# Kernel optimization log

Hardware: AMD Instinct MI355X
Metric: run time of the kernel (lower is better)

## Reference

```python
import jax, jax.numpy as jnp
import numpy as np

DIM = 2048
N_HEADS = 16
N_KV_HEADS = 8
HEAD_DIM = DIM // N_HEADS  # 128
N_REP = N_HEADS // N_KV_HEADS  # 2
HIDDEN = 4 * DIM  # Project hidden dim
SEQ = 2048
BSZ = 2
ROPE_THETA = 10000.0
NEG_INF = -1e9


def setup_inputs() -> dict:
    key = jax.random.key(0)
    ks = jax.random.split(key, 10)
    s_in = 1.0 / np.sqrt(DIM)
    s_hid = 1.0 / np.sqrt(HIDDEN)
    x = jax.random.normal(ks[0], (BSZ, SEQ, DIM), jnp.float32)
    wq = jax.random.normal(ks[1], (DIM, N_HEADS * HEAD_DIM), jnp.float32) * s_in
    wk_w1 = jax.random.normal(ks[2], (DIM, HIDDEN), jnp.float32) * s_in
    wk_w2 = jax.random.normal(ks[3], (HIDDEN, N_KV_HEADS * HEAD_DIM), jnp.float32) * s_hid
    wk_w3 = jax.random.normal(ks[4], (DIM, HIDDEN), jnp.float32) * s_in
    wv_w1 = jax.random.normal(ks[5], (DIM, HIDDEN), jnp.float32) * s_in
    wv_w2 = jax.random.normal(ks[6], (HIDDEN, N_KV_HEADS * HEAD_DIM), jnp.float32) * s_hid
    wv_w3 = jax.random.normal(ks[7], (DIM, HIDDEN), jnp.float32) * s_in
    wo = jax.random.normal(ks[8], (N_HEADS * HEAD_DIM, DIM), jnp.float32) * s_in
    # RoPE tables: angle[t, j] = t * theta^(-2j/head_dim), j in [0, head_dim/2)
    inv_freq = 1.0 / (ROPE_THETA ** (np.arange(0, HEAD_DIM, 2, dtype=np.float64) / HEAD_DIM))
    ang = np.outer(np.arange(SEQ, dtype=np.float64), inv_freq)
    freqs_cos = jnp.asarray(np.cos(ang), jnp.float32)  # [SEQ, HEAD_DIM//2]
    freqs_sin = jnp.asarray(np.sin(ang), jnp.float32)
    # causal additive mask [1, 1, SEQ, SEQ]
    mask = jnp.triu(jnp.full((SEQ, SEQ), NEG_INF, jnp.float32), k=1)[None, None]
    return {
        "x": x, "wq": wq,
        "wk_w1": wk_w1, "wk_w2": wk_w2, "wk_w3": wk_w3,
        "wv_w1": wv_w1, "wv_w2": wv_w2, "wv_w3": wv_w3,
        "wo": wo, "freqs_cos": freqs_cos, "freqs_sin": freqs_sin,
        "mask": mask, "start_pos": 0,
    }


def _rope(x, cos, sin):
    # x: [b, s, h, d]; pairs (x[2j], x[2j+1]) rotated as complex multiply
    xr = x[..., 0::2]
    xi = x[..., 1::2]
    c = cos[None, :, None, :]
    s = sin[None, :, None, :]
    out_r = xr * c - xi * s
    out_i = xr * s + xi * c
    return jnp.stack([out_r, out_i], axis=-1).reshape(x.shape)


def _project(x, w1, w2, w3):
    # SwiGLU-style projection: w2(silu(x@w1) * (x@w3))
    return (jax.nn.silu(x @ w1) * (x @ w3)) @ w2


def reference(x, wq, wk_w1, wk_w2, wk_w3, wv_w1, wv_w2, wv_w3, wo,
              freqs_cos, freqs_sin, mask, start_pos):
    b, s, _ = x.shape
    q = (x @ wq).reshape(b, s, N_HEADS, HEAD_DIM)
    q = _rope(q, freqs_cos, freqs_sin)
    k = _project(x, wk_w1, wk_w2, wk_w3).reshape(b, s, N_KV_HEADS, HEAD_DIM)
    v = _project(x, wv_w1, wv_w2, wv_w3).reshape(b, s, N_KV_HEADS, HEAD_DIM)
    k = _rope(k, freqs_cos, freqs_sin)
    o_keys, o_values = k, v  # is_training=True path: cache is just current k/v
    # repeat_kv (GQA) -> [b, h, s, d]
    kr = jnp.repeat(k, N_REP, axis=2).transpose(0, 2, 1, 3)
    vr = jnp.repeat(v, N_REP, axis=2).transpose(0, 2, 1, 3)
    qt = q.transpose(0, 2, 1, 3)
    scores = jnp.einsum('bhqd,bhkd->bhqk', qt, kr) / np.sqrt(HEAD_DIM).astype(np.float32)
    scores = scores + mask
    attn = jax.nn.softmax(scores.astype(jnp.float32), axis=-1).astype(qt.dtype)
    out = jnp.einsum('bhqk,bhkd->bhqd', attn, vr)
    out = out.transpose(0, 2, 1, 3).reshape(b, s, N_HEADS * HEAD_DIM)
    return (out @ wo, o_keys, o_values)
```

## Files before the change

### kernel.cpp

```cpp
#include <hip/hip_runtime.h>

typedef unsigned short ushort_t;
typedef __attribute__((ext_vector_type(4))) float f32x4;
typedef __attribute__((ext_vector_type(8))) __bf16 bf16x8;
typedef __attribute__((ext_vector_type(4))) unsigned short ushort4_t;
typedef __attribute__((ext_vector_type(8))) unsigned short ushort8_t;
typedef __attribute__((ext_vector_type(2))) unsigned int u32x2;

#define AS1 __attribute__((address_space(1)))
#define AS3 __attribute__((address_space(3)))

__device__ __forceinline__ float bf2f(ushort_t u) {
  unsigned int v = ((unsigned int)u) << 16;
  return __builtin_bit_cast(float, v);
}
__device__ __forceinline__ ushort_t f2bf(float f) {
  unsigned int u = __builtin_bit_cast(unsigned int, f);
  u += 0x7fffu + ((u >> 16) & 1u);
  return (ushort_t)(u >> 16);
}
__device__ __forceinline__ void storeC(float* p, float v) { *p = v; }
__device__ __forceinline__ void storeC(ushort_t* p, float v) { *p = f2bf(v); }

__global__ __launch_bounds__(256) void cast_f32_bf16(const float* __restrict__ in,
                                                     ushort_t* __restrict__ outp) {
  size_t i = ((size_t)blockIdx.x * 256 + threadIdx.x) * 4;
  f32x4 v = *(const f32x4*)(const void*)&in[i];
  ushort4_t o;
#pragma unroll
  for (int j = 0; j < 4; ++j) o[j] = f2bf(v[j]);
  *(ushort4_t*)(void*)&outp[i] = o;
}

__global__ __launch_bounds__(256) void transpose_cast_b(
    const float* __restrict__ W0, const float* __restrict__ W1,
    const float* __restrict__ W2, const float* __restrict__ W3,
    ushort_t* __restrict__ Wt, int K, int N, long long strT) {
  __shared__ float tile[32][33];
  const int z = blockIdx.z;
  const float* W = (z == 0) ? W0 : (z == 1) ? W1 : (z == 2) ? W2 : W3;
  ushort_t* out = Wt + (size_t)(strT * z);
  int n0 = blockIdx.x * 32, k0 = blockIdx.y * 32;
  int tx = threadIdx.x, ty = threadIdx.y;
#pragma unroll
  for (int i = 0; i < 4; ++i)
    tile[ty + 8 * i][tx] = W[(size_t)(k0 + ty + 8 * i) * N + n0 + tx];
  __syncthreads();
#pragma unroll
  for (int i = 0; i < 4; ++i)
    out[(size_t)(n0 + ty + 8 * i) * K + k0 + tx] = f2bf(tile[tx][ty + 8 * i]);
}

__global__ __launch_bounds__(256) void silu_mul(ushort_t* __restrict__ h1,
                                                const ushort_t* __restrict__ h3) {
  size_t i = ((size_t)blockIdx.x * 256 + threadIdx.x) * 8;
  ushort8_t a = *(const ushort8_t*)(const void*)&h1[i];
  ushort8_t b = *(const ushort8_t*)(const void*)&h3[i];
#pragma unroll
  for (int j = 0; j < 8; ++j) {
    float x = bf2f(a[j]);
    float g = x / (1.0f + __expf(-x));
    a[j] = f2bf(g * bf2f(b[j]));
  }
  *(ushort8_t*)(void*)&h1[i] = a;
}

__global__ __launch_bounds__(256) void reduce_q(const float* __restrict__ part,
                                                ushort_t* __restrict__ qb,
                                                const float* __restrict__ fc,
                                                const float* __restrict__ fs) {
  const float alpha = 0.08838834764831845f;
  int p = blockIdx.x * 256 + threadIdx.x;
  int i = p & 63;
  int h = (p >> 6) & 15;
  int row = p >> 10;
  int s = row & 2047;
  size_t src = (size_t)row * 2048 + h * 128 + 2 * i;
  float xr = part[src] + part[src + 8388608];
  float xi = part[src + 1] + part[src + 8388609];
  float c = fc[s * 64 + i] * alpha, sn = fs[s * 64 + i] * alpha;
  qb[src] = f2bf(xr * c - xi * sn);
  qb[src + 1] = f2bf(xr * sn + xi * c);
}

__global__ __launch_bounds__(256) void reduce_k(const float* __restrict__ part,
                                                ushort_t* __restrict__ kb,
                                                float* __restrict__ okeys,
                                                const float* __restrict__ fc,
                                                const float* __restrict__ fs) {
  int p = blockIdx.x * 256 + threadIdx.x;
  int i = p & 63;
  int kh = (p >> 6) & 7;
  int row = p >> 9;
  int s = row & 2047;
  size_t src = (size_t)row * 1024 + kh * 128 + 2 * i;
  float xr = part[src] + part[src + 4194304] + part[src + 8388608] + part[src + 12582912];
  float xi = part[src + 1] + part[src + 1 + 4194304] + part[src + 1 + 8388608] +
             part[src + 1 + 12582912];
  float c = fc[s * 64 + i], sn = fs[s * 64 + i];
  float orr = xr * c - xi * sn;
  float oi = xr * sn + xi * c;
  kb[src] = f2bf(orr);
  kb[src + 1] = f2bf(oi);
  okeys[src] = orr;
  okeys[src + 1] = oi;
}

__global__ __launch_bounds__(256) void reduce_v(const float* __restrict__ part,
                                                float* __restrict__ ovals,
                                                ushort_t* __restrict__ vbT) {
  __shared__ ushort_t tile[32][33];
  int s0 = blockIdx.x * 32, d0 = blockIdx.y * 32, bk = blockIdx.z;
  int b = bk >> 3, kh = bk & 7;
  int tx = threadIdx.x, ty = threadIdx.y;
#pragma unroll
  for (int i = 0; i < 4; ++i) {
    int s = s0 + ty + 8 * i;
    size_t src = ((size_t)(b * 2048 + s)) * 1024 + kh * 128 + d0 + tx;
    float v = part[src] + part[src + 4194304] + part[src + 8388608] + part[src + 12582912];
    tile[ty + 8 * i][tx] = f2bf(v);
    ovals[src] = v;
  }
  __syncthreads();
#pragma unroll
  for (int i = 0; i < 4; ++i) {
    int d = d0 + ty + 8 * i;
    vbT[((size_t)bk * 128 + d) * 2048 + s0 + tx] = tile[tx][ty + 8 * i];
  }
}

__global__ __launch_bounds__(256) void reduce_wo(const float* __restrict__ part,
                                                 float* __restrict__ outp) {
  size_t i = ((size_t)blockIdx.x * 256 + threadIdx.x) * 4;
  f32x4 a = *(const f32x4*)(const void*)&part[i];
  f32x4 b = *(const f32x4*)(const void*)&part[i + 8388608];
  *(f32x4*)(void*)&outp[i] = a + b;
}

__global__ __launch_bounds__(256) void flash_attn(
    const ushort_t* __restrict__ Q, const ushort_t* __restrict__ Kg,
    const ushort_t* __restrict__ VT, ushort_t* __restrict__ O) {
  __shared__ __align__(16) char smem[81920];
  const int xp = blockIdx.x;
  const int bh = blockIdx.y;
  const int b = bh >> 4, h = bh & 15, kh = h >> 1;
  const int t = threadIdx.x, w = t >> 6, lane = t & 63;
  const int fr = lane & 15, fh = lane >> 4;
  const size_t kelem0 = ((size_t)b * 2048) * 1024 + kh * 128;
  const size_t velem0 = ((size_t)(b * 8 + kh)) * 128 * 2048;
  const size_t qrow0 = (size_t)b * 2048;

  size_t oK[4], oV[4];
#pragma unroll
  for (int qv = 0; qv < 4; ++qv) {
    int row = w * 16 + qv * 4 + (lane >> 4);
    oK[qv] = (size_t)row * 1024 + (((lane & 15) ^ (row & 7)) * 8);
    int rd = w * 32 + qv * 8 + (lane >> 3);
    oV[qv] = (size_t)rd * 2048 + (((lane & 7) ^ (rd & 7)) * 8);
  }

  auto stage = [&](int tile, int buf) {
    const size_t kc = (size_t)tile * 64 * 1024;
    const int vc = tile * 64;
    char* kd = smem + buf * 16384 + w * 4096;
    char* vd = smem + 32768 + buf * 16384 + w * 4096;
#pragma unroll
    for (int qv = 0; qv < 4; ++qv) {
      __builtin_amdgcn_global_load_lds((const AS1 void*)(Kg + kelem0 + kc + oK[qv]),
                                       (AS3 void*)(kd + qv * 1024), 16, 0, 0);
      __builtin_amdgcn_global_load_lds((const AS1 void*)(VT + velem0 + oV[qv] + vc),
                                       (AS3 void*)(vd + qv * 1024), 16, 0, 0);
    }
  };

#pragma unroll 1
  for (int ph = 0; ph < 2; ++ph) {
    const int qi = ph ? (15 - xp) : xp;
    const int qw = qi * 128 + w * 32;
    const int nt = 2 * qi + 2;

    bf16x8 qF[2][4];
#pragma unroll
    for (int qt = 0; qt < 2; ++qt)
#pragma unroll
      for (int i = 0; i < 4; ++i)
        qF[qt][i] = *(const bf16x8*)(const void*)(
            Q + (qrow0 + qw + qt * 16 + fr) * 2048 + h * 128 + i * 32 + fh * 8);

    f32x4 acco[8][2] = {};
    float mrun[2] = {-1e30f, -1e30f};
    float lrun[2] = {0.0f, 0.0f};

    stage(0, 0);
#pragma unroll 1
    for (int tt = 0; tt < nt; ++tt) {
      const int c0 = tt * 64;
      if (tt + 1 < nt) {
        stage(tt + 1, (tt + 1) & 1);
        asm volatile("s_waitcnt vmcnt(8)" ::: "memory");
      } else {
        asm volatile("s_waitcnt vmcnt(0)" ::: "memory");
      }
      __builtin_amdgcn_sched_barrier(0);
      __builtin_amdgcn_s_barrier();
      const char* KL = smem + (tt & 1) * 16384;
      const char* VL = smem + 32768 + (tt & 1) * 16384;
      char* PL = smem + 65536 + w * 4096;
      if (c0 <= qw + 31) {
        f32x4 sacc[2][4] = {};
#pragma unroll
        for (int i = 0; i < 4; ++i)
#pragma unroll
          for (int mt = 0; mt < 4; ++mt) {
            bf16x8 kf = *(const bf16x8*)(const void*)(
                KL + (mt * 16 + fr) * 256 + (((i * 4 + fh) ^ (fr & 7)) * 16));
            sacc[0][mt] = __builtin_amdgcn_mfma_f32_16x16x32_bf16(kf, qF[0][i], sacc[0][mt], 0, 0, 0);
            sacc[1][mt] = __builtin_amdgcn_mfma_f32_16x16x32_bf16(kf, qF[1][i], sacc[1][mt], 0, 0, 0);
          }
        if (c0 + 63 > qw) {
#pragma unroll
          for (int qt = 0; qt < 2; ++qt) {
            int qg = qw + qt * 16 + fr;
#pragma unroll
            for (int mt = 0; mt < 4; ++mt)
#pragma unroll
              for (int j = 0; j < 4; ++j)
                if (c0 + mt * 16 + fh * 4 + j > qg) sacc[qt][mt][j] = -1e30f;
          }
        }
#pragma unroll
        for (int qt = 0; qt < 2; ++qt) {
          float mt_ = -1e30f;
#pragma unroll
          for (int mt = 0; mt < 4; ++mt)
#pragma unroll
            for (int j = 0; j < 4; ++j) mt_ = fmaxf(mt_, sacc[qt][mt][j]);
          mt_ = fmaxf(mt_, __shfl_xor(mt_, 16, 64));
          mt_ = fmaxf(mt_, __shfl_xor(mt_, 32, 64));
          float mnew = fmaxf(mrun[qt], mt_);
          float corr = __expf(mrun[qt] - mnew);
          mrun[qt] = mnew;
          float ps = 0.0f;
          float pv[4][4];
#pragma unroll
          for (int mt = 0; mt < 4; ++mt)
#pragma unroll
            for (int j = 0; j < 4; ++j) {
              float pe = __expf(sacc[qt][mt][j] - mnew);
              pv[mt][j] = pe;
              ps += pe;
            }
          ps += __shfl_xor(ps, 16, 64);
          ps += __shfl_xor(ps, 32, 64);
          lrun[qt] = lrun[qt] * corr + ps;
#pragma unroll
          for (int mt = 0; mt < 4; ++mt) {
            unsigned int u0, u1;
            asm("v_cvt_pk_bf16_f32 %0, %1, %2" : "=v"(u0) : "v"(pv[mt][0]), "v"(pv[mt][1]));
            asm("v_cvt_pk_bf16_f32 %0, %1, %2" : "=v"(u1) : "v"(pv[mt][2]), "v"(pv[mt][3]));
            u32x2 val;
            val[0] = u0;
            val[1] = u1;
            *(u32x2*)(void*)(PL + qt * 2048 + fr * 128 +
                             (((2 * mt + (fh >> 1)) ^ (fr & 7)) * 16) + (fh & 1) * 8) = val;
          }
#pragma unroll
          for (int dt = 0; dt < 8; ++dt) acco[dt][qt] *= corr;
        }
        bf16x8 pf[2][2];
#pragma unroll
        for (int qt = 0; qt < 2; ++qt)
#pragma unroll
          for (int ks = 0; ks < 2; ++ks)
            pf[qt][ks] = *(const bf16x8*)(const void*)(
                PL + qt * 2048 + fr * 128 + (((ks * 4 + fh) ^ (fr & 7)) * 16));
#pragma unroll
        for (int dt = 0; dt < 8; ++dt)
#pragma unroll
          for (int ks = 0; ks < 2; ++ks) {
            bf16x8 vf = *(const bf16x8*)(const void*)(
                VL + (dt * 16 + fr) * 128 + (((ks * 4 + fh) ^ (fr & 7)) * 16));
            acco[dt][0] = __builtin_amdgcn_mfma_f32_16x16x32_bf16(vf, pf[0][ks], acco[dt][0], 0, 0, 0);
            acco[dt][1] = __builtin_amdgcn_mfma_f32_16x16x32_bf16(vf, pf[1][ks], acco[dt][1], 0, 0, 0);
          }
      }
      __builtin_amdgcn_s_barrier();
    }
#pragma unroll
    for (int qt = 0; qt < 2; ++qt) {
      float inv = 1.0f / lrun[qt];
      const size_t rb = (qrow0 + qw + qt * 16 + fr) * 2048 + h * 128;
#pragma unroll
      for (int dt = 0; dt < 8; ++dt) {
        ushort4_t o4;
#pragma unroll
        for (int j = 0; j < 4; ++j) o4[j] = f2bf(acco[dt][qt][j] * inv);
        *(ushort4_t*)(void*)(O + rb + dt * 16 + fh * 4) = o4;
      }
    }
  }
}

template <typename CT>
__global__ __launch_bounds__(512, 2) void gemm256(
    const ushort_t* __restrict__ A, const ushort_t* __restrict__ B,
    CT* __restrict__ C, int K, int lda, int ldb, int ldc,
    int nwgx, int nwg, long long strA, long long strB, long long strC) {
  __shared__ __align__(16) char smem[131072];
  const int bz = blockIdx.y;
  const int bid = blockIdx.x;
  const int swz = (bid & 7) * (nwg >> 3) + (bid >> 3);
  const int r0 = (swz / nwgx) * 256;
  const int c0 = (swz % nwgx) * 256;
  const int t = threadIdx.x, w = t >> 6, lane = t & 63;
  const int wm = w >> 2, wn = w & 3;
  const int fr = lane & 15, fh = lane >> 4;
  const int sl0 = (fh ^ (fr & 7)) << 4;
  const int ldsw = w * 1024;
  const int srow = t >> 3;
  const int scb = (t & 7) ^ (srow & 7);
  const int NT = K >> 6;
  const ushort_t* gA = A + strA * bz + (size_t)(r0 + srow) * lda + scb * 8;
  const ushort_t* gB = B + strB * bz + (size_t)(c0 + srow) * ldb + scb * 8;

  auto stage = [&](int tile, int isB, int h) {
    const ushort_t* g = isB ? gB : gA;
    const size_t ld = isB ? (size_t)ldb : (size_t)lda;
    char* lp = (char*)smem + ((tile & 1) << 16) + (isB ? 32768 : 0) + (h << 14) + ldsw;
    const ushort_t* src = g + (size_t)(h * 128) * ld + tile * 64;
    __builtin_amdgcn_global_load_lds((const AS1 void*)src, (AS3 void*)lp, 16, 0, 0);
    __builtin_amdgcn_global_load_lds((const AS1 void*)(src + 64 * ld),
                                     (AS3 void*)(lp + 8192), 16, 0, 0);
  };

  f32x4 acc[8][4] = {};

  stage(0, 0, 0); stage(0, 0, 1); stage(0, 1, 0); stage(0, 1, 1);
  if (NT > 1) {
    stage(1, 0, 0); stage(1, 0, 1); stage(1, 1, 0); stage(1, 1, 1);
    asm volatile("s_waitcnt vmcnt(8)" ::: "memory");
  } else {
    asm volatile("s_waitcnt vmcnt(0)" ::: "memory");
  }
  __builtin_amdgcn_sched_barrier(0);
  __builtin_amdgcn_s_barrier();

  const int aOff = wm * 16384 + fr * 128;
  const int bOff = 32768 + wn * 8192 + fr * 128;

  for (int kt = 0; kt < NT; ++kt) {
    const int buf = (kt & 1) << 16;
    const char* la = (const char*)smem + buf + aOff;
    const char* lb = (const char*)smem + buf + bOff;
    bf16x8 aF0[8], aF1[8], bF0[4], bF1[4];
#pragma unroll
    for (int m = 0; m < 8; ++m)
      aF0[m] = *(const bf16x8*)(const void*)(la + m * 2048 + sl0);
#pragma unroll
    for (int n = 0; n < 4; ++n)
      bF0[n] = *(const bf16x8*)(const void*)(lb + n * 2048 + sl0);
    __builtin_amdgcn_s_barrier();
    asm volatile("s_waitcnt lgkmcnt(0)" ::: "memory");
    __builtin_amdgcn_sched_barrier(0);
    __builtin_amdgcn_s_setprio(1);
#pragma unroll
    for (int m = 0; m < 4; ++m)
#pragma unroll
      for (int n = 0; n < 4; ++n)
        acc[m][n] = __builtin_amdgcn_mfma_f32_16x16x32_bf16(aF0[m], bF0[n], acc[m][n], 0, 0, 0);
    __builtin_amdgcn_s_setprio(0);
    __builtin_amdgcn_s_barrier();
#pragma unroll
    for (int m = 0; m < 8; ++m)
      aF1[m] = *(const bf16x8*)(const void*)(la + m * 2048 + (sl0 ^ 64));
#pragma unroll
    for (int n = 0; n < 4; ++n)
      bF1[n] = *(const bf16x8*)(const void*)(lb + n * 2048 + (sl0 ^ 64));
    __builtin_amdgcn_s_barrier();
    asm volatile("s_waitcnt lgkmcnt(0)" ::: "memory");
    __builtin_amdgcn_sched_barrier(0);
    __builtin_amdgcn_s_setprio(1);
#pragma unroll
    for (int m = 4; m < 8; ++m)
#pragma unroll
      for (int n = 0; n < 4; ++n)
        acc[m][n] = __builtin_amdgcn_mfma_f32_16x16x32_bf16(aF0[m], bF0[n], acc[m][n], 0, 0, 0);
    __builtin_amdgcn_s_setprio(0);
    __builtin_amdgcn_s_barrier();
    if (kt + 2 < NT) { stage(kt + 2, 0, 0); stage(kt + 2, 1, 0); }
    __builtin_amdgcn_s_barrier();
    __builtin_amdgcn_s_setprio(1);
#pragma unroll
    for (int m = 0; m < 4; ++m)
#pragma unroll
      for (int n = 0; n < 4; ++n)
        acc[m][n] = __builtin_amdgcn_mfma_f32_16x16x32_bf16(aF1[m], bF1[n], acc[m][n], 0, 0, 0);
    __builtin_amdgcn_s_setprio(0);
    __builtin_amdgcn_s_barrier();
    if (kt + 2 < NT) { stage(kt + 2, 0, 1); stage(kt + 2, 1, 1); }
    __builtin_amdgcn_s_setprio(1);
#pragma unroll
    for (int m = 4; m < 8; ++m)
#pragma unroll
      for (int n = 0; n < 4; ++n)
        acc[m][n] = __builtin_amdgcn_mfma_f32_16x16x32_bf16(aF1[m], bF1[n], acc[m][n], 0, 0, 0);
    __builtin_amdgcn_s_setprio(0);
    if (kt + 2 < NT)
      asm volatile("s_waitcnt vmcnt(8)" ::: "memory");
    else if (kt + 1 < NT)
      asm volatile("s_waitcnt vmcnt(0)" ::: "memory");
    __builtin_amdgcn_sched_barrier(0);
    __builtin_amdgcn_s_barrier();
  }

  CT* gC = C + strC * bz;
  const int cr = r0 + wm * 128 + fh * 4;
  const int cc = c0 + wn * 64 + fr;
#pragma unroll
  for (int m = 0; m < 8; ++m)
#pragma unroll
    for (int n = 0; n < 4; ++n)
#pragma unroll
      for (int j = 0; j < 4; ++j)
        storeC(&gC[(size_t)(cr + m * 16 + j) * ldc + cc + n * 16], acc[m][n][j]);
}

extern "C" void kernel_launch(void* const* d_in, const int* in_sizes, int n_in,
                              void* d_out, int out_size, void* d_ws, size_t ws_size,
                              hipStream_t stream) {
  const float* x = (const float*)d_in[0];
  const float* wq = (const float*)d_in[1];
  const float* wk1 = (const float*)d_in[2];
  const float* wk2 = (const float*)d_in[3];
  const float* wk3 = (const float*)d_in[4];
  const float* wv1 = (const float*)d_in[5];
  const float* wv2 = (const float*)d_in[6];
  const float* wv3 = (const float*)d_in[7];
  const float* wo = (const float*)d_in[8];
  const float* fc = (const float*)d_in[9];
  const float* fs = (const float*)d_in[10];

  float* outp = (float*)d_out;
  float* okeys = outp + 8388608;
  float* ovals = outp + 12582912;

  char* p = (char*)d_ws;
  auto alloc = [&](size_t bytes) {
    char* r = p;
    p += (bytes + 255) & ~(size_t)255;
    return r;
  };
  ushort_t* xb = (ushort_t*)alloc(8388608ull * 2);
  ushort_t* w4T = (ushort_t*)alloc(4ull * 16777216 * 2);
  ushort_t* w2T = (ushort_t*)alloc(2ull * 8388608 * 2);
  ushort_t* wqoT = (ushort_t*)alloc(2ull * 4194304 * 2);
  ushort_t* qb = (ushort_t*)alloc(8388608ull * 2);
  ushort_t* kb = (ushort_t*)alloc(4194304ull * 2);
  ushort_t* vbT = (ushort_t*)alloc(4194304ull * 2);
  ushort_t* ob = (ushort_t*)alloc(8388608ull * 2);
  char* hreg = alloc(134217728ull);
  ushort_t* h1 = (ushort_t*)hreg;
  float* part67 = (float*)(hreg + 67108864);
  float* partQO = (float*)hreg;

  ushort_t* wk1T = w4T;
  ushort_t* wk2T = w2T;
  ushort_t* wv1T = w4T + 2ull * 16777216;
  ushort_t* wv2T = w2T + 8388608;
  ushort_t* wqT = wqoT;
  ushort_t* woT = wqoT + 4194304;

  dim3 tb(32, 8);

  cast_f32_bf16<<<8192, 256, 0, stream>>>(x, xb);
  transpose_cast_b<<<dim3(256, 64, 4), tb, 0, stream>>>(wk1, wk3, wv1, wv3, w4T,
                                                        2048, 8192, 16777216);
  transpose_cast_b<<<dim3(32, 256, 2), tb, 0, stream>>>(wk2, wv2, wk2, wv2, w2T,
                                                        8192, 1024, 8388608);
  transpose_cast_b<<<dim3(64, 64, 2), tb, 0, stream>>>(wq, wo, wq, wo, wqoT,
                                                       2048, 2048, 4194304);

  gemm256<float><<<dim3(128, 2), 512, 0, stream>>>(
      xb, wqT, partQO, 1024, 2048, 2048, 2048, 8, 128, 1024, 1024, 8388608);
  reduce_q<<<16384, 256, 0, stream>>>(partQO, qb, fc, fs);

  gemm256<ushort_t><<<dim3(512, 2), 512, 0, stream>>>(
      xb, wk1T, h1, 2048, 2048, 2048, 8192, 32, 512, 0, 16777216, 33554432);
  silu_mul<<<16384, 256, 0, stream>>>(h1, h1 + 33554432);
  gemm256<float><<<dim3(64, 4), 512, 0, stream>>>(
      h1, wk2T, part67, 2048, 8192, 8192, 1024, 4, 64, 2048, 2048, 4194304);
  reduce_k<<<8192, 256, 0, stream>>>(part67, kb, okeys, fc, fs);

  gemm256<ushort_t><<<dim3(512, 2), 512, 0, stream>>>(
      xb, wv1T, h1, 2048, 2048, 2048, 8192, 32, 512, 0, 16777216, 33554432);
  silu_mul<<<16384, 256, 0, stream>>>(h1, h1 + 33554432);
  gemm256<float><<<dim3(64, 4), 512, 0, stream>>>(
      h1, wv2T, part67, 2048, 8192, 8192, 1024, 4, 64, 2048, 2048, 4194304);
  reduce_v<<<dim3(64, 4, 16), tb, 0, stream>>>(part67, ovals, vbT);

  flash_attn<<<dim3(8, 32), 256, 0, stream>>>(qb, kb, vbT, ob);

  gemm256<float><<<dim3(128, 2), 512, 0, stream>>>(
      ob, woT, partQO, 1024, 2048, 2048, 2048, 8, 128, 1024, 1024, 8388608);
  reduce_wo<<<8192, 256, 0, stream>>>(partQO, outp);

  (void)in_sizes; (void)n_in; (void)out_size; (void)ws_size;
}
```

Measured before the change: 1.048 ms.

## Restructure gemm256 pipeline to prefetch one tile ahead with split fragment loads

The gemm256 main loop now issues the next tile's global-to-LDS loads at the start of each iteration (prefetch distance one instead of two). The LDS layout is regrouped so A and B each get their own double-buffered region. Register fragments are split into smaller aL/aH/bb sets that are reloaded per quarter step, which is meant to lower register pressure and raise occupancy. The cost is less latency hiding, since loads have only one iteration to land, plus extra LDS reads and waits per iteration. Small index simplifications in reduce_q/reduce_k do not change behaviour.

```diff
diff --git a/kernel.cpp b/kernel.cpp
--- a/kernel.cpp
+++ b/kernel.cpp
@@ -72,10 +72,9 @@
   const float alpha = 0.08838834764831845f;
   int p = blockIdx.x * 256 + threadIdx.x;
   int i = p & 63;
-  int h = (p >> 6) & 15;
   int row = p >> 10;
   int s = row & 2047;
-  size_t src = (size_t)row * 2048 + h * 128 + 2 * i;
+  size_t src = (size_t)row * 2048 + ((p >> 6) & 15) * 128 + 2 * i;
   float xr = part[src] + part[src + 8388608];
   float xi = part[src + 1] + part[src + 8388609];
   float c = fc[s * 64 + i] * alpha, sn = fs[s * 64 + i] * alpha;
@@ -90,10 +89,9 @@
                                                 const float* __restrict__ fs) {
   int p = blockIdx.x * 256 + threadIdx.x;
   int i = p & 63;
-  int kh = (p >> 6) & 7;
   int row = p >> 9;
   int s = row & 2047;
-  size_t src = (size_t)row * 1024 + kh * 128 + 2 * i;
+  size_t src = (size_t)row * 1024 + ((p >> 6) & 7) * 128 + 2 * i;
   float xr = part[src] + part[src + 4194304] + part[src + 8388608] + part[src + 12582912];
   float xi = part[src + 1] + part[src + 1 + 4194304] + part[src + 1 + 8388608] +
              part[src + 1 + 12582912];
@@ -315,7 +313,7 @@
   const int t = threadIdx.x, w = t >> 6, lane = t & 63;
   const int wm = w >> 2, wn = w & 3;
   const int fr = lane & 15, fh = lane >> 4;
-  const int sl0 = (fh ^ (fr & 7)) << 4;
+  const int sl = (fh ^ (fr & 7)) << 4;
   const int ldsw = w * 1024;
   const int srow = t >> 3;
   const int scb = (t & 7) ^ (srow & 7);
@@ -326,7 +324,7 @@
   auto stage = [&](int tile, int isB, int h) {
     const ushort_t* g = isB ? gB : gA;
     const size_t ld = isB ? (size_t)ldb : (size_t)lda;
-    char* lp = (char*)smem + ((tile & 1) << 16) + (isB ? 32768 : 0) + (h << 14) + ldsw;
+    char* lp = (char*)smem + (isB ? 65536 : 0) + ((tile & 1) << 15) + (h << 14) + ldsw;
     const ushort_t* src = g + (size_t)(h * 128) * ld + tile * 64;
     __builtin_amdgcn_global_load_lds((const AS1 void*)src, (AS3 void*)lp, 16, 0, 0);
     __builtin_amdgcn_global_load_lds((const AS1 void*)(src + 64 * ld),
@@ -335,30 +333,26 @@
 
   f32x4 acc[8][4] = {};
 
-  stage(0, 0, 0); stage(0, 0, 1); stage(0, 1, 0); stage(0, 1, 1);
-  if (NT > 1) {
-    stage(1, 0, 0); stage(1, 0, 1); stage(1, 1, 0); stage(1, 1, 1);
-    asm volatile("s_waitcnt vmcnt(8)" ::: "memory");
-  } else {
-    asm volatile("s_waitcnt vmcnt(0)" ::: "memory");
-  }
+  stage(0, 0, 0); stage(0, 1, 0); stage(0, 0, 1); stage(0, 1, 1);
+  asm volatile("s_waitcnt vmcnt(0)" ::: "memory");
   __builtin_amdgcn_sched_barrier(0);
   __builtin_amdgcn_s_barrier();
 
-  const int aOff = wm * 16384 + fr * 128;
-  const int bOff = 32768 + wn * 8192 + fr * 128;
+  const int aBase = wm * 16384 + fr * 128;
+  const int bBase = 65536 + wn * 8192 + fr * 128;
 
   for (int kt = 0; kt < NT; ++kt) {
-    const int buf = (kt & 1) << 16;
-    const char* la = (const char*)smem + buf + aOff;
-    const char* lb = (const char*)smem + buf + bOff;
-    bf16x8 aF0[8], aF1[8], bF0[4], bF1[4];
-#pragma unroll
-    for (int m = 0; m < 8; ++m)
-      aF0[m] = *(const bf16x8*)(const void*)(la + m * 2048 + sl0);
+    const int buf = (kt & 1) << 15;
+    const char* la = (const char*)smem + buf + aBase;
+    const char* lb = (const char*)smem + buf + bBase;
+    bf16x8 aL[4], aH[4], bb[4];
+#pragma unroll
+    for (int m = 0; m < 4; ++m)
+      aL[m] = *(const bf16x8*)(const void*)(la + m * 2048 + sl);
 #pragma unroll
     for (int n = 0; n < 4; ++n)
-      bF0[n] = *(const bf16x8*)(const void*)(lb + n * 2048 + sl0);
+      bb[n] = *(const bf16x8*)(const void*)(lb + n * 2048 + sl);
+    if (kt + 1 < NT) { stage(kt + 1, 0, 0); stage(kt + 1, 1, 0); }
     __builtin_amdgcn_s_barrier();
     asm volatile("s_waitcnt lgkmcnt(0)" ::: "memory");
     __builtin_amdgcn_sched_barrier(0);
@@ -367,47 +361,55 @@
     for (int m = 0; m < 4; ++m)
 #pragma unroll
       for (int n = 0; n < 4; ++n)
-        acc[m][n] = __builtin_amdgcn_mfma_f32_16x16x32_bf16(aF0[m], bF0[n], acc[m][n], 0, 0, 0);
+        acc[m][n] = __builtin_amdgcn_mfma_f32_16x16x32_bf16(aL[m], bb[n], acc[m][n], 0, 0, 0);
     __builtin_amdgcn_s_setprio(0);
     __builtin_amdgcn_s_barrier();
 #pragma unroll
-    for (int m = 0; m < 8; ++m)
-      aF1[m] = *(const bf16x8*)(const void*)(la + m * 2048 + (sl0 ^ 64));
-#pragma unroll
-    for (int n = 0; n < 4; ++n)
-      bF1[n] = *(const bf16x8*)(const void*)(lb + n * 2048 + (sl0 ^ 64));
+    for (int m = 0; m < 4; ++m)
+      aH[m] = *(const bf16x8*)(const void*)(la + (m + 4) * 2048 + sl);
+    if (kt + 1 < NT) { stage(kt + 1, 0, 1); stage(kt + 1, 1, 1); }
     __builtin_amdgcn_s_barrier();
     asm volatile("s_waitcnt lgkmcnt(0)" ::: "memory");
     __builtin_amdgcn_sched_barrier(0);
     __builtin_amdgcn_s_setprio(1);
 #pragma unroll
-    for (int m = 4; m < 8; ++m)
+    for (int m = 0; m < 4; ++m)
 #pragma unroll
       for (int n = 0; n < 4; ++n)
-        acc[m][n] = __builtin_amdgcn_mfma_f32_16x16x32_bf16(aF0[m], bF0[n], acc[m][n], 0, 0, 0);
+        acc[m + 4][n] = __builtin_amdgcn_mfma_f32_16x16x32_bf16(aH[m], bb[n], acc[m + 4][n], 0, 0, 0);
     __builtin_amdgcn_s_setprio(0);
     __builtin_amdgcn_s_barrier();
-    if (kt + 2 < NT) { stage(kt + 2, 0, 0); stage(kt + 2, 1, 0); }
-    __builtin_amdgcn_s_barrier();
+#pragma unroll
+    for (int m = 0; m < 4; ++m)
+      aL[m] = *(const bf16x8*)(const void*)(la + m * 2048 + (sl ^ 64));
+#pragma unroll
+    for (int n = 0; n < 4; ++n)
+      bb[n] = *(const bf16x8*)(const void*)(lb + n * 2048 + (sl ^ 64));
+    __builtin_amdgcn_s_barrier();
+    asm volatile("s_waitcnt lgkmcnt(0)" ::: "memory");
+    __builtin_amdgcn_sched_barrier(0);
     __builtin_amdgcn_s_setprio(1);
 #pragma unroll
     for (int m = 0; m < 4; ++m)
 #pragma unroll
       for (int n = 0; n < 4; ++n)
-        acc[m][n] = __builtin_amdgcn_mfma_f32_16x16x32_bf16(aF1[m], bF1[n], acc[m][n], 0, 0, 0);
+        acc[m][n] = __builtin_amdgcn_mfma_f32_16x16x32_bf16(aL[m], bb[n], acc[m][n], 0, 0, 0);
     __builtin_amdgcn_s_setprio(0);
     __builtin_amdgcn_s_barrier();
-    if (kt + 2 < NT) { stage(kt + 2, 0, 1); stage(kt + 2, 1, 1); }
+#pragma unroll
+    for (int m = 0; m < 4; ++m)
+      aH[m] = *(const bf16x8*)(const void*)(la + (m + 4) * 2048 + (sl ^ 64));
+    __builtin_amdgcn_s_barrier();
+    asm volatile("s_waitcnt lgkmcnt(0)" ::: "memory");
+    __builtin_amdgcn_sched_barrier(0);
     __builtin_amdgcn_s_setprio(1);
 #pragma unroll
-    for (int m = 4; m < 8; ++m)
+    for (int m = 0; m < 4; ++m)
 #pragma unroll
       for (int n = 0; n < 4; ++n)
-        acc[m][n] = __builtin_amdgcn_mfma_f32_16x16x32_bf16(aF1[m], bF1[n], acc[m][n], 0, 0, 0);
+        acc[m + 4][n] = __builtin_amdgcn_mfma_f32_16x16x32_bf16(aH[m], bb[n], acc[m + 4][n], 0, 0, 0);
     __builtin_amdgcn_s_setprio(0);
-    if (kt + 2 < NT)
-      asm volatile("s_waitcnt vmcnt(8)" ::: "memory");
-    else if (kt + 1 < NT)
+    if (kt + 1 < NT)
       asm volatile("s_waitcnt vmcnt(0)" ::: "memory");
     __builtin_amdgcn_sched_barrier(0);
     __builtin_amdgcn_s_barrier();
```

Measured after the change: 1.050 ms. No clear change (+0.2%).
